# Optimization experiments

Hardware: AMD Instinct MI355X
Metric: run time of the kernel (lower is better)

## Reference

```python
import jax, jax.numpy as jnp
import numpy as np

B, N, D_IN = 8, 2048, 1024
H, DH = 4, 256  # num_heads, per-head dim (hidden_dim)
D_OUT = 256


def setup_inputs() -> dict:
    key = jax.random.key(0)
    ks = jax.random.split(key, 5)
    s = 0.02
    return {
        "x": jax.random.normal(ks[0], (B, N, D_IN), dtype=jnp.float32),
        "Wq": jax.random.normal(ks[1], (D_IN, H * DH), dtype=jnp.float32) * s,
        "bq": jnp.zeros((H * DH,), dtype=jnp.float32),
        "Wk": jax.random.normal(ks[2], (D_IN, H * DH), dtype=jnp.float32) * s,
        "bk": jnp.zeros((H * DH,), dtype=jnp.float32),
        "Wv": jax.random.normal(ks[3], (D_IN, H * DH), dtype=jnp.float32) * s,
        "bv": jnp.zeros((H * DH,), dtype=jnp.float32),
        "Wo": jax.random.normal(ks[4], (H * DH, D_OUT), dtype=jnp.float32) * s,
        "bo": jnp.zeros((D_OUT,), dtype=jnp.float32),
    }


def reference(x, Wq, bq, Wk, bk, Wv, bv, Wo, bo):
    b, n, _ = x.shape
    # projections -> [B, N, H, DH]
    q = (x @ Wq + bq).reshape(b, n, H, DH)
    k = (x @ Wk + bk).reshape(b, n, H, DH)
    v = (x @ Wv + bv).reshape(b, n, H, DH)
    scale = 1.0 / jnp.sqrt(jnp.asarray(DH, dtype=x.dtype))
    scores = jnp.einsum("bnhd,bmhd->bhnm", q, k) * scale  # [B,H,N,N]
    weights = jax.nn.softmax(scores, axis=-1)
    attn = jnp.einsum("bhnm,bmhd->bnhd", weights, v)  # [B,N,H,DH]
    attn = attn.reshape(b, n, H * DH)
    return attn @ Wo + bo  # [B, N, D_OUT]
```

## Files before the change

kernel.cpp:

```cpp
#include <hip/hip_runtime.h>
#include <hip/hip_bf16.h>
#include <stdint.h>

typedef __attribute__((ext_vector_type(4)))  float  f32x4;
typedef __attribute__((ext_vector_type(16))) float  f32x16;
typedef __attribute__((ext_vector_type(4)))  float  float4v;
typedef __attribute__((ext_vector_type(8)))  short  short8v;
typedef __attribute__((ext_vector_type(4)))  short  short4v;
typedef __attribute__((ext_vector_type(8)))  unsigned short ushort8v;
typedef __attribute__((ext_vector_type(4)))  unsigned short ushort4v;

#define B_   8
#define N_   2048
#define DIN  1024
#define H_   4
#define DH   256
#define QSZ  (B_ * N_ * H_ * DH)

__device__ __forceinline__ unsigned short f2bf(float x) {
  union { float f; unsigned u; } v; v.f = x;
  unsigned r = v.u + 0x7fffu + ((v.u >> 16) & 1u);
  return (unsigned short)(r >> 16);
}

__device__ __forceinline__ unsigned cvtpk(float lo, float hi) {
  unsigned r;
  asm("v_cvt_pk_bf16_f32 %0, %1, %2" : "=v"(r) : "v"(lo), "v"(hi));
  return r;
}

__device__ __forceinline__ void gload_lds16(const void* g, void* l) {
  __builtin_amdgcn_global_load_lds(
      (const __attribute__((address_space(1))) unsigned int*)g,
      (__attribute__((address_space(3))) unsigned int*)l, 16, 0, 0);
}

__global__ __launch_bounds__(256) void prep_wt(
    const float* __restrict__ Wq, const float* __restrict__ Wk,
    const float* __restrict__ Wv, const float* __restrict__ Wo,
    unsigned short* __restrict__ Wt)
{
  __shared__ float Lt[64][68];
  const int tid = threadIdx.x;
  const int c0 = blockIdx.x * 64;
  const int k0 = blockIdx.y * 64;
  const int msel = c0 >> 10;
  const float* src = (msel == 0) ? Wq : (msel == 1) ? Wk : (msel == 2) ? Wv : Wo;
  const int stride = (msel == 3) ? 256 : 1024;
  const int cloc = c0 - msel * 1024;
  #pragma unroll
  for (int p = 0; p < 4; ++p) {
    int kr = p * 16 + (tid >> 4), c4 = (tid & 15) * 4;
    float4v v = *(const float4v*)(src + (size_t)(k0 + kr) * stride + cloc + c4);
    Lt[kr][c4 + 0] = v[0]; Lt[kr][c4 + 1] = v[1];
    Lt[kr][c4 + 2] = v[2]; Lt[kr][c4 + 3] = v[3];
  }
  __syncthreads();
  int n = tid >> 2, kc = (tid & 3) * 16;
  ushort8v h0, h1;
  #pragma unroll
  for (int j = 0; j < 8; ++j) h0[j] = f2bf(Lt[kc + j][n]);
  #pragma unroll
  for (int j = 0; j < 8; ++j) h1[j] = f2bf(Lt[kc + 8 + j][n]);
  unsigned short* dst = Wt + (size_t)(c0 + n) * 1024 + k0 + kc;
  *(ushort8v*)dst = h0;
  *(ushort8v*)(dst + 8) = h1;
}

__global__ __launch_bounds__(512) void qkv_gemm2(
    const float* __restrict__ x, const unsigned short* __restrict__ Wt,
    const float* __restrict__ bq, const float* __restrict__ bk,
    const float* __restrict__ bv, unsigned short* __restrict__ qkv)
{
  __shared__ __align__(16) unsigned short Ab[2][4096];
  __shared__ __align__(16) unsigned short Bb[2][8192];
  const int tid = threadIdx.x;
  const int lane = tid & 63, wid = tid >> 6;
  const int l15 = lane & 15, l4 = lane >> 4;

  const int id = blockIdx.x;
  const int swz = (id & 7) * 192 + (id >> 3);
  const int m0 = (swz / 12) * 128, n0 = (swz % 12) * 256;
  const int wm = (wid >> 2) * 64, wn = (wid & 3) * 64;

  const int arow = tid >> 2, akb = (tid & 3) * 16;
  const int brow1 = wid * 16 + (lane >> 2), bkb = (lane & 3) * 16;
  const float* Abase = x + (size_t)(m0 + arow) * 1024 + (akb >> 1);
  const char* Bg1 = (const char*)Wt + (size_t)(n0 + brow1) * 2048 + bkb;
  const char* Bg2 = Bg1 + 128 * 2048;

  f32x4 acc[4][4] = {};

#define QSTAGE(t, b) do {                                                    \
    float4v f0 = *(const float4v*)(Abase + (t) * 32);                        \
    float4v f1 = *(const float4v*)(Abase + (t) * 32 + 4);                    \
    gload_lds16(Bg1 + (t) * 64, (char*)&Bb[b][0] + wid * 1024);              \
    gload_lds16(Bg2 + (t) * 64, (char*)&Bb[b][0] + 8192 + wid * 1024);       \
    ushort8v hv;                                                             \
    hv[0] = f2bf(f0[0]); hv[1] = f2bf(f0[1]);                                \
    hv[2] = f2bf(f0[2]); hv[3] = f2bf(f0[3]);                                \
    hv[4] = f2bf(f1[0]); hv[5] = f2bf(f1[1]);                                \
    hv[6] = f2bf(f1[2]); hv[7] = f2bf(f1[3]);                                \
    *(ushort8v*)((char*)&Ab[b][0] + tid * 16) = hv;                          \
  } while (0)

  QSTAGE(0, 0);
  __syncthreads();

  for (int t = 0; t < 32; ++t) {
    const int cur = t & 1;
    if (t < 31) QSTAGE(t + 1, cur ^ 1);
    short8v a[4], b[4];
    #pragma unroll
    for (int mf = 0; mf < 4; ++mf)
      a[mf] = *(const short8v*)((const char*)&Ab[cur][0] +
                                (wm + mf * 16 + l15) * 64 + l4 * 16);
    #pragma unroll
    for (int nf = 0; nf < 4; ++nf)
      b[nf] = *(const short8v*)((const char*)&Bb[cur][0] +
                                (wn + nf * 16 + l15) * 64 + l4 * 16);
    #pragma unroll
    for (int mf = 0; mf < 4; ++mf)
      #pragma unroll
      for (int nf = 0; nf < 4; ++nf)
        acc[mf][nf] = __builtin_amdgcn_mfma_f32_16x16x32_bf16(a[mf], b[nf], acc[mf][nf], 0, 0, 0);
    __syncthreads();
  }
#undef QSTAGE

  const int wsel = n0 >> 10;
  const float* bias = (wsel == 0) ? bq : (wsel == 1) ? bk : bv;
  if (wsel == 2) {
    unsigned short* vt = qkv + (size_t)2 * QSZ;
    #pragma unroll
    for (int nf = 0; nf < 4; ++nf) {
      int ncl = (n0 + wn + nf * 16 + l15) & 1023;
      float bv_ = bias[ncl];
      int h = ncl >> 8, d = ncl & 255;
      #pragma unroll
      for (int mf = 0; mf < 4; ++mf) {
        int mrow0 = m0 + wm + mf * 16 + l4 * 4;
        int bb = mrow0 >> 11, nn0 = mrow0 & 2047;
        ushort4v o;
        #pragma unroll
        for (int e = 0; e < 4; ++e) o[e] = f2bf(acc[mf][nf][e] + bv_);
        *(ushort4v*)&vt[((size_t)((bb * 4 + h) * 256 + d)) * 2048 + nn0] = o;
      }
    }
  } else {
    const float scale = (wsel == 0) ? 0.0625f * 1.44269504f : 1.0f;
    unsigned short* dst = qkv + (size_t)wsel * QSZ;
    #pragma unroll
    for (int nf = 0; nf < 4; ++nf) {
      int ncl = (n0 + wn + nf * 16 + l15) & 1023;
      float bv_ = bias[ncl];
      int h = ncl >> 8, d = ncl & 255;
      #pragma unroll
      for (int mf = 0; mf < 4; ++mf)
        #pragma unroll
        for (int e = 0; e < 4; ++e) {
          int mrow = m0 + wm + mf * 16 + l4 * 4 + e;
          int bb = mrow >> 11, nn = mrow & 2047;
          dst[((size_t)(bb * 4 + h) * 2048 + nn) * 256 + d] =
              f2bf((acc[mf][nf][e] + bv_) * scale);
        }
    }
  }
}

__global__ __launch_bounds__(512, 2) void attn_fused(
    unsigned short* __restrict__ qkv)
{
  extern __shared__ __align__(16) char smem[];
  const int tid = threadIdx.x;
  const int lane = tid & 63, wid = tid >> 6;
  const int l31 = lane & 31, hi = lane >> 5;

  const int id0 = blockIdx.x;
  const int swzb = (id0 & 7) * 32 + (id0 >> 3);
  const int qt = swzb & 7, bh = swzb >> 3;

  const unsigned short* Qh = qkv + (size_t)bh * (N_ * DH);
  const unsigned short* Kh = qkv + (size_t)QSZ + (size_t)bh * (N_ * DH);
  const unsigned short* Vt = qkv + (size_t)2 * QSZ + (size_t)bh * (N_ * DH);

  const int q0 = qt * 256 + wid * 32;
  short8v qf[16];
  #pragma unroll
  for (int st = 0; st < 16; ++st)
    qf[st] = *(const short8v*)(Qh + (size_t)(q0 + l31) * DH + st * 16 + hi * 8);

  const int skv = tid >> 3, sks = tid & 7;
  const unsigned short* Kg = Kh + (size_t)skv * DH + sks * 8;
  int kdst[4];
  #pragma unroll
  for (int g = 0; g < 4; ++g)
    kdst[g] = skv * 512 + (((g * 8 + sks) ^ (skv & 7)) << 4);

  int vgoff[4];
  #pragma unroll
  for (int j = 0; j < 4; ++j) {
    int r = j * 64 + wid * 8 + (lane >> 3);
    int u = lane & 7;
    vgoff[j] = r * 4096 + ((u ^ (r & 7)) << 4);
  }

  const int dswz = (l31 & 7) << 4;
  const int krow0 = l31 * 512;
  int vbs[4];
  #pragma unroll
  for (int s = 0; s < 4; ++s)
    vbs[s] = l31 * 128 + (((s * 2 + hi) ^ (l31 & 7)) << 4);

  f32x16 ot[8] = {};
  float mr = -1.0e30f, lp = 0.0f;

  ushort8v kin0, kin1, kin2, kin3;

#define KBUF(b) (smem + (b) * 32768)
#define VBUF(b) (smem + 65536 + (b) * 32768)
#define BMF32 __builtin_amdgcn_mfma_f32_32x32x16_bf16

#define KISSUE(t) do {                                                       \
    const unsigned short* kp = Kg + (size_t)(t) * (64 * DH);                 \
    kin0 = *(const ushort8v*)(kp);                                           \
    kin1 = *(const ushort8v*)(kp + 64);                                      \
    kin2 = *(const ushort8v*)(kp + 128);                                     \
    kin3 = *(const ushort8v*)(kp + 192);                                     \
  } while (0)

#define KWRITE(b) do {                                                       \
    char* kb = KBUF(b);                                                      \
    *(ushort8v*)(kb + kdst[0]) = kin0;                                       \
    *(ushort8v*)(kb + kdst[1]) = kin1;                                       \
    *(ushort8v*)(kb + kdst[2]) = kin2;                                       \
    *(ushort8v*)(kb + kdst[3]) = kin3;                                       \
  } while (0)

#define VISSUE(t, b) do {                                                    \
    const char* vg = (const char*)Vt + (size_t)(t) * 128;                    \
    _Pragma("unroll")                                                        \
    for (int j = 0; j < 4; ++j)                                              \
      gload_lds16(vg + vgoff[j], VBUF(b) + j * 8192 + wid * 1024);           \
  } while (0)

  union UPK { unsigned u[4]; short8v v; };

  KISSUE(0);
  VISSUE(0, 0);
  KWRITE(0);
  __syncthreads();

  for (int t = 0; t < 32; ++t) {
    const int cur = t & 1;
    if (t < 31) VISSUE(t + 1, cur ^ 1);

    const char* Kc = KBUF(cur);
    f32x16 sa = {}, sb = {};
    __builtin_amdgcn_s_setprio(1);
    #pragma unroll
    for (int st = 0; st < 16; ++st) {
      int off = (st * 32 + hi * 16) ^ dswz;
      short8v a0 = *(const short8v*)(Kc + krow0 + off);
      short8v a1 = *(const short8v*)(Kc + 16384 + krow0 + off);
      sa = BMF32(a0, qf[st], sa, 0, 0, 0);
      sb = BMF32(a1, qf[st], sb, 0, 0, 0);
    }
    __builtin_amdgcn_s_setprio(0);

    if (t < 31) KISSUE(t + 1);

    float tm = sa[0];
    #pragma unroll
    for (int i = 1; i < 16; ++i) tm = fmaxf(tm, sa[i]);
    #pragma unroll
    for (int i = 0; i < 16; ++i) tm = fmaxf(tm, sb[i]);
    tm = fmaxf(tm, __shfl_xor(tm, 32));
    if (__any(tm > mr + 11.54f)) {
      float mn = fmaxf(mr, tm), al = exp2f(mr - mn);
      lp *= al;
      #pragma unroll
      for (int df = 0; df < 8; ++df) ot[df] *= al;
      mr = mn;
    }
    #pragma unroll
    for (int i = 0; i < 16; ++i) { sa[i] = exp2f(sa[i] - mr); sb[i] = exp2f(sb[i] - mr); }
    #pragma unroll
    for (int i = 0; i < 16; ++i) lp += sa[i] + sb[i];

    short8v pb0, pb1, pb2, pb3;
    {
      unsigned x0 = cvtpk(sa[0], sa[1]),  y0 = cvtpk(sa[4], sa[5]);
      unsigned x1 = cvtpk(sa[2], sa[3]),  y1 = cvtpk(sa[6], sa[7]);
      unsigned x2 = cvtpk(sa[8], sa[9]),  y2 = cvtpk(sa[12], sa[13]);
      unsigned x3 = cvtpk(sa[10], sa[11]), y3 = cvtpk(sa[14], sa[15]);
      asm("v_permlane32_swap_b32 %0, %1" : "+v"(x0), "+v"(y0));
      asm("v_permlane32_swap_b32 %0, %1" : "+v"(x1), "+v"(y1));
      asm("v_permlane32_swap_b32 %0, %1" : "+v"(x2), "+v"(y2));
      asm("v_permlane32_swap_b32 %0, %1" : "+v"(x3), "+v"(y3));
      UPK u0; u0.u[0] = x0; u0.u[1] = x1; u0.u[2] = y0; u0.u[3] = y1; pb0 = u0.v;
      UPK u1; u1.u[0] = x2; u1.u[1] = x3; u1.u[2] = y2; u1.u[3] = y3; pb1 = u1.v;
    }
    {
      unsigned x0 = cvtpk(sb[0], sb[1]),  y0 = cvtpk(sb[4], sb[5]);
      unsigned x1 = cvtpk(sb[2], sb[3]),  y1 = cvtpk(sb[6], sb[7]);
      unsigned x2 = cvtpk(sb[8], sb[9]),  y2 = cvtpk(sb[12], sb[13]);
      unsigned x3 = cvtpk(sb[10], sb[11]), y3 = cvtpk(sb[14], sb[15]);
      asm("v_permlane32_swap_b32 %0, %1" : "+v"(x0), "+v"(y0));
      asm("v_permlane32_swap_b32 %0, %1" : "+v"(x1), "+v"(y1));
      asm("v_permlane32_swap_b32 %0, %1" : "+v"(x2), "+v"(y2));
      asm("v_permlane32_swap_b32 %0, %1" : "+v"(x3), "+v"(y3));
      UPK u0; u0.u[0] = x0; u0.u[1] = x1; u0.u[2] = y0; u0.u[3] = y1; pb2 = u0.v;
      UPK u1; u1.u[0] = x2; u1.u[1] = x3; u1.u[2] = y2; u1.u[3] = y3; pb3 = u1.v;
    }

    const char* Vc = VBUF(cur);
    __builtin_amdgcn_s_setprio(1);
    #pragma unroll
    for (int df = 0; df < 8; ++df) {
      const char* vr = Vc + df * 4096;
      short8v v0 = *(const short8v*)(vr + vbs[0]);
      short8v v1 = *(const short8v*)(vr + vbs[1]);
      short8v v2 = *(const short8v*)(vr + vbs[2]);
      short8v v3 = *(const short8v*)(vr + vbs[3]);
      ot[df] = BMF32(v0, pb0, ot[df], 0, 0, 0);
      ot[df] = BMF32(v1, pb1, ot[df], 0, 0, 0);
      ot[df] = BMF32(v2, pb2, ot[df], 0, 0, 0);
      ot[df] = BMF32(v3, pb3, ot[df], 0, 0, 0);
    }
    __builtin_amdgcn_s_setprio(0);

    if (t < 31) KWRITE(cur ^ 1);

    __syncthreads();
  }

  lp += __shfl_xor(lp, 32);
  float inv = 1.0f / lp;
  unsigned short* Oq = (unsigned short*)Qh;
  size_t base = (size_t)(q0 + l31) * DH;
  #pragma unroll
  for (int df = 0; df < 8; ++df) {
    #pragma unroll
    for (int j = 0; j < 4; ++j) {
      int d = df * 32 + j * 8 + hi * 4;
      ushort4v o;
      #pragma unroll
      for (int e = 0; e < 4; ++e) o[e] = f2bf(ot[df][j * 4 + e] * inv);
      *(ushort4v*)&Oq[base + d] = o;
    }
  }
#undef KISSUE
#undef KWRITE
#undef VISSUE
#undef KBUF
#undef VBUF
#undef BMF32
}

__global__ __launch_bounds__(256) void out_gemm3(
    const unsigned short* __restrict__ Aq, const unsigned short* __restrict__ WoT,
    const float* __restrict__ bo, float* __restrict__ out)
{
  __shared__ __align__(16) unsigned short Ab[2][2048];
  __shared__ __align__(16) unsigned short Bb[2][8192];
  const int tid = threadIdx.x;
  const int lane = tid & 63, wid = tid >> 6;
  const int l15 = lane & 15, l4 = lane >> 4;
  const int m0 = blockIdx.x * 64;
  const int wn = wid * 64;
  const int bb = m0 >> 11;
  const int qbase = m0 & 2047;
  const int sr = lane >> 2, sc = lane & 3;

  f32x4 acc[4][4] = {};

#define OSTAGE(t, b) do {                                                    \
    int h = (t) >> 3;                                                        \
    int d0 = ((t) & 7) * 32 + sc * 8;                                        \
    gload_lds16(Aq + ((size_t)(bb * 4 + h) * 2048 + qbase + wid * 16 + sr)   \
                         * 256 + d0,                                         \
                (char*)&Ab[b][0] + wid * 1024);                              \
    _Pragma("unroll")                                                        \
    for (int i = 0; i < 4; ++i) {                                            \
      int br = wid * 64 + i * 16 + sr;                                       \
      gload_lds16((const char*)WoT + (size_t)br * 2048 + (t) * 64 + sc * 16, \
                  (char*)&Bb[b][0] + (wid * 4 + i) * 1024);                  \
    }                                                                        \
  } while (0)

  OSTAGE(0, 0);
  __syncthreads();

  for (int t = 0; t < 32; ++t) {
    const int cur = t & 1;
    if (t < 31) OSTAGE(t + 1, cur ^ 1);
    short8v a[4], b[4];
    #pragma unroll
    for (int mf = 0; mf < 4; ++mf)
      a[mf] = *(const short8v*)((const char*)&Ab[cur][0] +
                                (mf * 16 + l15) * 64 + l4 * 16);
    #pragma unroll
    for (int nf = 0; nf < 4; ++nf)
      b[nf] = *(const short8v*)((const char*)&Bb[cur][0] +
                                (wn + nf * 16 + l15) * 64 + l4 * 16);
    #pragma unroll
    for (int mf = 0; mf < 4; ++mf)
      #pragma unroll
      for (int nf = 0; nf < 4; ++nf)
        acc[mf][nf] = __builtin_amdgcn_mfma_f32_16x16x32_bf16(a[mf], b[nf], acc[mf][nf], 0, 0, 0);
    __syncthreads();
  }
#undef OSTAGE

  #pragma unroll
  for (int nf = 0; nf < 4; ++nf) {
    int ncol = wn + nf * 16 + l15;
    float bv_ = bo[ncol];
    #pragma unroll
    for (int mf = 0; mf < 4; ++mf)
      #pragma unroll
      for (int e = 0; e < 4; ++e) {
        int mrow = m0 + mf * 16 + l4 * 4 + e;
        out[(size_t)mrow * 256 + ncol] = acc[mf][nf][e] + bv_;
      }
  }
}

extern "C" void kernel_launch(void* const* d_in, const int* in_sizes, int n_in,
                              void* d_out, int out_size, void* d_ws, size_t ws_size,
                              hipStream_t stream) {
  const float* x  = (const float*)d_in[0];
  const float* Wq = (const float*)d_in[1];
  const float* bq = (const float*)d_in[2];
  const float* Wk = (const float*)d_in[3];
  const float* bk = (const float*)d_in[4];
  const float* Wv = (const float*)d_in[5];
  const float* bv = (const float*)d_in[6];
  const float* Wo = (const float*)d_in[7];
  const float* bo = (const float*)d_in[8];

  unsigned short* qkvbuf = (unsigned short*)d_ws;
  unsigned short* Wt     = qkvbuf + (size_t)3 * QSZ;
  float* out = (float*)d_out;

  prep_wt  <<<dim3(52, 16), 256, 0, stream>>>(Wq, Wk, Wv, Wo, Wt);
  qkv_gemm2<<<dim3(1536),   512, 0, stream>>>(x, Wt, bq, bk, bv, qkvbuf);
  attn_fused<<<dim3(256),   512, 131072, stream>>>(qkvbuf);
  out_gemm3<<<dim3(256),    256, 0, stream>>>(qkvbuf, Wt + (size_t)3072 * 1024, bo, out);
}
```

Baseline: 366.8 us.

## Software-pipeline attention loop by overlapping previous tile's PV with current QK

Restructures the flash-attention main loop so each iteration's P·V MFMA block uses the probabilities and V buffer from the previous tile. That block is issued right after the current tile's Q·K^T MFMAs. The K/V global-to-LDS staging for the next tile is moved after a new mid-iteration barrier, and one PV block is drained after the loop. The goal is to give the matrix cores a long, independent run of work while the softmax of the current tile happens, hiding exp and conversion latency. In exchange it adds a second __syncthreads per iteration and keeps the packed P registers live across iterations, which raises register pressure.

```diff
diff --git a/kernel.cpp b/kernel.cpp
--- a/kernel.cpp
+++ b/kernel.cpp
@@ -214,6 +214,7 @@
 
   f32x16 ot[8] = {};
   float mr = -1.0e30f, lp = 0.0f;
+  short8v pb0 = {}, pb1 = {}, pb2 = {}, pb3 = {};
 
   ushort8v kin0, kin1, kin2, kin3;
 
@@ -244,6 +245,21 @@
       gload_lds16(vg + vgoff[j], VBUF(b) + j * 8192 + wid * 1024);           \
   } while (0)
 
+#define PVBLOCK(Vc) do {                                                     \
+    _Pragma("unroll")                                                        \
+    for (int df = 0; df < 8; ++df) {                                         \
+      const char* vr = (Vc) + df * 4096;                                     \
+      short8v v0 = *(const short8v*)(vr + vbs[0]);                           \
+      short8v v1 = *(const short8v*)(vr + vbs[1]);                           \
+      short8v v2 = *(const short8v*)(vr + vbs[2]);                           \
+      short8v v3 = *(const short8v*)(vr + vbs[3]);                           \
+      ot[df] = BMF32(v0, pb0, ot[df], 0, 0, 0);                              \
+      ot[df] = BMF32(v1, pb1, ot[df], 0, 0, 0);                              \
+      ot[df] = BMF32(v2, pb2, ot[df], 0, 0, 0);                              \
+      ot[df] = BMF32(v3, pb3, ot[df], 0, 0, 0);                              \
+    }                                                                        \
+  } while (0)
+
   union UPK { unsigned u[4]; short8v v; };
 
   KISSUE(0);
@@ -253,7 +269,7 @@
 
   for (int t = 0; t < 32; ++t) {
     const int cur = t & 1;
-    if (t < 31) VISSUE(t + 1, cur ^ 1);
+    if (t < 31) KISSUE(t + 1);
 
     const char* Kc = KBUF(cur);
     f32x16 sa = {}, sb = {};
@@ -266,9 +282,15 @@
       sa = BMF32(a0, qf[st], sa, 0, 0, 0);
       sb = BMF32(a1, qf[st], sb, 0, 0, 0);
     }
+    if (t > 0) PVBLOCK(VBUF(cur ^ 1));
     __builtin_amdgcn_s_setprio(0);
 
-    if (t < 31) KISSUE(t + 1);
+    __syncthreads();
+
+    if (t < 31) {
+      KWRITE(cur ^ 1);
+      VISSUE(t + 1, cur ^ 1);
+    }
 
     float tm = sa[0];
     #pragma unroll
@@ -288,7 +310,6 @@
     #pragma unroll
     for (int i = 0; i < 16; ++i) lp += sa[i] + sb[i];
 
-    short8v pb0, pb1, pb2, pb3;
     {
       unsigned x0 = cvtpk(sa[0], sa[1]),  y0 = cvtpk(sa[4], sa[5]);
       unsigned x1 = cvtpk(sa[2], sa[3]),  y1 = cvtpk(sa[6], sa[7]);
@@ -314,26 +335,12 @@
       UPK u1; u1.u[0] = x2; u1.u[1] = x3; u1.u[2] = y2; u1.u[3] = y3; pb3 = u1.v;
     }
 
-    const char* Vc = VBUF(cur);
-    __builtin_amdgcn_s_setprio(1);
-    #pragma unroll
-    for (int df = 0; df < 8; ++df) {
-      const char* vr = Vc + df * 4096;
-      short8v v0 = *(const short8v*)(vr + vbs[0]);
-      short8v v1 = *(const short8v*)(vr + vbs[1]);
-      short8v v2 = *(const short8v*)(vr + vbs[2]);
-      short8v v3 = *(const short8v*)(vr + vbs[3]);
-      ot[df] = BMF32(v0, pb0, ot[df], 0, 0, 0);
-      ot[df] = BMF32(v1, pb1, ot[df], 0, 0, 0);
-      ot[df] = BMF32(v2, pb2, ot[df], 0, 0, 0);
-      ot[df] = BMF32(v3, pb3, ot[df], 0, 0, 0);
-    }
-    __builtin_amdgcn_s_setprio(0);
-
-    if (t < 31) KWRITE(cur ^ 1);
-
     __syncthreads();
   }
+
+  __builtin_amdgcn_s_setprio(1);
+  PVBLOCK(VBUF(1));
+  __builtin_amdgcn_s_setprio(0);
 
   lp += __shfl_xor(lp, 32);
   float inv = 1.0f / lp;
@@ -353,6 +360,7 @@
 #undef KISSUE
 #undef KWRITE
 #undef VISSUE
+#undef PVBLOCK
 #undef KBUF
 #undef VBUF
 #undef BMF32
```

Result: slower. 480.7 us (+31.0%).

## Halve attention tile sizes: 4-wave blocks, 128-query tiles, 32-key KV steps

Applied to the files above, without the earlier changes.

Restructures the fused attention kernel from 8-wave blocks covering 256 queries with 64-key K/V tiles to 4-wave blocks covering 128 queries with 32-key tiles. LDS use drops from 128KB to 64KB per block and the grid doubles to 512 blocks, so two blocks can share a CU and blocks are finer-grained for scheduling. In exchange, each K/V tile is reused by half as many queries, so global K/V traffic doubles, and the loop runs 64 iterations with a barrier each instead of 32, leaving less MFMA work per sync to hide load latency.

```diff
diff --git a/kernel.cpp b/kernel.cpp
--- a/kernel.cpp
+++ b/kernel.cpp
@@ -168,7 +168,7 @@
   }
 }
 
-__global__ __launch_bounds__(512, 2) void attn_fused(
+__global__ __launch_bounds__(256, 2) void attn_fused(
     unsigned short* __restrict__ qkv)
 {
   extern __shared__ __align__(16) char smem[];
@@ -177,14 +177,14 @@
   const int l31 = lane & 31, hi = lane >> 5;
 
   const int id0 = blockIdx.x;
-  const int swzb = (id0 & 7) * 32 + (id0 >> 3);
-  const int qt = swzb & 7, bh = swzb >> 3;
+  const int swzb = (id0 & 7) * 64 + (id0 >> 3);
+  const int qt = swzb & 15, bh = swzb >> 4;
 
   const unsigned short* Qh = qkv + (size_t)bh * (N_ * DH);
   const unsigned short* Kh = qkv + (size_t)QSZ + (size_t)bh * (N_ * DH);
   const unsigned short* Vt = qkv + (size_t)2 * QSZ + (size_t)bh * (N_ * DH);
 
-  const int q0 = qt * 256 + wid * 32;
+  const int q0 = qt * 128 + wid * 32;
   short8v qf[16];
   #pragma unroll
   for (int st = 0; st < 16; ++st)
@@ -200,29 +200,29 @@
   int vgoff[4];
   #pragma unroll
   for (int j = 0; j < 4; ++j) {
-    int r = j * 64 + wid * 8 + (lane >> 3);
-    int u = lane & 7;
-    vgoff[j] = r * 4096 + ((u ^ (r & 7)) << 4);
+    int r = j * 64 + (tid >> 2);
+    int u = tid & 3;
+    vgoff[j] = r * 4096 + ((u ^ (r & 3)) << 4);
   }
 
   const int dswz = (l31 & 7) << 4;
   const int krow0 = l31 * 512;
-  int vbs[4];
-  #pragma unroll
-  for (int s = 0; s < 4; ++s)
-    vbs[s] = l31 * 128 + (((s * 2 + hi) ^ (l31 & 7)) << 4);
+  int vbs[2];
+  #pragma unroll
+  for (int s = 0; s < 2; ++s)
+    vbs[s] = l31 * 64 + (((s * 2 + hi) ^ (l31 & 3)) << 4);
 
   f32x16 ot[8] = {};
   float mr = -1.0e30f, lp = 0.0f;
 
   ushort8v kin0, kin1, kin2, kin3;
 
-#define KBUF(b) (smem + (b) * 32768)
-#define VBUF(b) (smem + 65536 + (b) * 32768)
+#define KBUF(b) (smem + (b) * 16384)
+#define VBUF(b) (smem + 32768 + (b) * 16384)
 #define BMF32 __builtin_amdgcn_mfma_f32_32x32x16_bf16
 
 #define KISSUE(t) do {                                                       \
-    const unsigned short* kp = Kg + (size_t)(t) * (64 * DH);                 \
+    const unsigned short* kp = Kg + (size_t)(t) * (32 * DH);                 \
     kin0 = *(const ushort8v*)(kp);                                           \
     kin1 = *(const ushort8v*)(kp + 64);                                      \
     kin2 = *(const ushort8v*)(kp + 128);                                     \
@@ -238,10 +238,10 @@
   } while (0)
 
 #define VISSUE(t, b) do {                                                    \
-    const char* vg = (const char*)Vt + (size_t)(t) * 128;                    \
+    const char* vg = (const char*)Vt + (size_t)(t) * 64;                     \
     _Pragma("unroll")                                                        \
     for (int j = 0; j < 4; ++j)                                              \
-      gload_lds16(vg + vgoff[j], VBUF(b) + j * 8192 + wid * 1024);           \
+      gload_lds16(vg + vgoff[j], VBUF(b) + j * 4096 + tid * 16);             \
   } while (0)
 
   union UPK { unsigned u[4]; short8v v; };
@@ -251,30 +251,26 @@
   KWRITE(0);
   __syncthreads();
 
-  for (int t = 0; t < 32; ++t) {
+  for (int t = 0; t < 64; ++t) {
     const int cur = t & 1;
-    if (t < 31) VISSUE(t + 1, cur ^ 1);
+    if (t < 63) VISSUE(t + 1, cur ^ 1);
 
     const char* Kc = KBUF(cur);
-    f32x16 sa = {}, sb = {};
+    f32x16 sa = {};
     __builtin_amdgcn_s_setprio(1);
     #pragma unroll
     for (int st = 0; st < 16; ++st) {
       int off = (st * 32 + hi * 16) ^ dswz;
       short8v a0 = *(const short8v*)(Kc + krow0 + off);
-      short8v a1 = *(const short8v*)(Kc + 16384 + krow0 + off);
       sa = BMF32(a0, qf[st], sa, 0, 0, 0);
-      sb = BMF32(a1, qf[st], sb, 0, 0, 0);
     }
     __builtin_amdgcn_s_setprio(0);
 
-    if (t < 31) KISSUE(t + 1);
+    if (t < 63) KISSUE(t + 1);
 
     float tm = sa[0];
     #pragma unroll
     for (int i = 1; i < 16; ++i) tm = fmaxf(tm, sa[i]);
-    #pragma unroll
-    for (int i = 0; i < 16; ++i) tm = fmaxf(tm, sb[i]);
     tm = fmaxf(tm, __shfl_xor(tm, 32));
     if (__any(tm > mr + 11.54f)) {
       float mn = fmaxf(mr, tm), al = exp2f(mr - mn);
@@ -284,11 +280,11 @@
       mr = mn;
     }
     #pragma unroll
-    for (int i = 0; i < 16; ++i) { sa[i] = exp2f(sa[i] - mr); sb[i] = exp2f(sb[i] - mr); }
-    #pragma unroll
-    for (int i = 0; i < 16; ++i) lp += sa[i] + sb[i];
-
-    short8v pb0, pb1, pb2, pb3;
+    for (int i = 0; i < 16; ++i) sa[i] = exp2f(sa[i] - mr);
+    #pragma unroll
+    for (int i = 0; i < 16; ++i) lp += sa[i];
+
+    short8v pb0, pb1;
     {
       unsigned x0 = cvtpk(sa[0], sa[1]),  y0 = cvtpk(sa[4], sa[5]);
       unsigned x1 = cvtpk(sa[2], sa[3]),  y1 = cvtpk(sa[6], sa[7]);
@@ -301,36 +297,20 @@
       UPK u0; u0.u[0] = x0; u0.u[1] = x1; u0.u[2] = y0; u0.u[3] = y1; pb0 = u0.v;
       UPK u1; u1.u[0] = x2; u1.u[1] = x3; u1.u[2] = y2; u1.u[3] = y3; pb1 = u1.v;
     }
-    {
-      unsigned x0 = cvtpk(sb[0], sb[1]),  y0 = cvtpk(sb[4], sb[5]);
-      unsigned x1 = cvtpk(sb[2], sb[3]),  y1 = cvtpk(sb[6], sb[7]);
-      unsigned x2 = cvtpk(sb[8], sb[9]),  y2 = cvtpk(sb[12], sb[13]);
-      unsigned x3 = cvtpk(sb[10], sb[11]), y3 = cvtpk(sb[14], sb[15]);
-      asm("v_permlane32_swap_b32 %0, %1" : "+v"(x0), "+v"(y0));
-      asm("v_permlane32_swap_b32 %0, %1" : "+v"(x1), "+v"(y1));
-      asm("v_permlane32_swap_b32 %0, %1" : "+v"(x2), "+v"(y2));
-      asm("v_permlane32_swap_b32 %0, %1" : "+v"(x3), "+v"(y3));
-      UPK u0; u0.u[0] = x0; u0.u[1] = x1; u0.u[2] = y0; u0.u[3] = y1; pb2 = u0.v;
-      UPK u1; u1.u[0] = x2; u1.u[1] = x3; u1.u[2] = y2; u1.u[3] = y3; pb3 = u1.v;
-    }
 
     const char* Vc = VBUF(cur);
     __builtin_amdgcn_s_setprio(1);
     #pragma unroll
     for (int df = 0; df < 8; ++df) {
-      const char* vr = Vc + df * 4096;
+      const char* vr = Vc + df * 2048;
       short8v v0 = *(const short8v*)(vr + vbs[0]);
       short8v v1 = *(const short8v*)(vr + vbs[1]);
-      short8v v2 = *(const short8v*)(vr + vbs[2]);
-      short8v v3 = *(const short8v*)(vr + vbs[3]);
       ot[df] = BMF32(v0, pb0, ot[df], 0, 0, 0);
       ot[df] = BMF32(v1, pb1, ot[df], 0, 0, 0);
-      ot[df] = BMF32(v2, pb2, ot[df], 0, 0, 0);
-      ot[df] = BMF32(v3, pb3, ot[df], 0, 0, 0);
     }
     __builtin_amdgcn_s_setprio(0);
 
-    if (t < 31) KWRITE(cur ^ 1);
+    if (t < 63) KWRITE(cur ^ 1);
 
     __syncthreads();
   }
@@ -446,6 +426,6 @@
 
   prep_wt  <<<dim3(52, 16), 256, 0, stream>>>(Wq, Wk, Wv, Wo, Wt);
   qkv_gemm2<<<dim3(1536),   512, 0, stream>>>(x, Wt, bq, bk, bv, qkvbuf);
-  attn_fused<<<dim3(256),   512, 131072, stream>>>(qkvbuf);
+  attn_fused<<<dim3(512),   256, 65536, stream>>>(qkvbuf);
   out_gemm3<<<dim3(256),    256, 0, stream>>>(qkvbuf, Wt + (size_t)3072 * 1024, bo, out);
 }
```

New measurement: 340.5 us. 7.2% less time.
